# Performance work log

Hardware: AMD Instinct MI355X
Metric: run time of the kernel (lower is better)

Reference implementation:

```python
import jax, jax.numpy as jnp
import numpy as np

N = 30000   # nodes
E = 300000  # edges
B = 64      # graphs
H = 4       # heads
C = 64      # channels per head
HC = H * C  # 256


def setup_inputs() -> dict:
    key = jax.random.key(0)
    ks = jax.random.split(key, 32)

    def rn(k, shape):
        scale = 1.0 / np.sqrt(shape[0])
        return (jax.random.normal(k, shape) * scale).astype(jnp.float32)

    inp = {}
    inp["x"] = jax.random.normal(ks[0], (N, 13), dtype=jnp.float32)
    inp["edge_index"] = jax.random.randint(ks[1], (2, E), 0, N, dtype=jnp.int64)
    inp["edge_attr"] = jax.random.normal(ks[2], (E, 51), dtype=jnp.float32)
    inp["batch"] = jnp.sort(jax.random.randint(ks[3], (N,), 0, B, dtype=jnp.int64))
    # init node MLP: Linear(13 -> 128) (plain_last => no act/norm)
    inp["W0"] = rn(ks[4], (13, 128)); inp["b0"] = jnp.zeros((128,), jnp.float32)
    # GATv2 layer 1: in 128 -> H=4, C=64
    inp["Wl1"] = rn(ks[5], (128, HC)); inp["bl1"] = jnp.zeros((HC,), jnp.float32)
    inp["Wr1"] = rn(ks[6], (128, HC)); inp["br1"] = jnp.zeros((HC,), jnp.float32)
    inp["We1"] = rn(ks[7], (51, HC))
    inp["att1"] = rn(ks[8], (H, C))
    inp["bias1"] = jnp.zeros((HC,), jnp.float32)
    # GATv2 layer 2: in 256 -> H=4, C=64
    inp["Wl2"] = rn(ks[9], (HC, HC)); inp["bl2"] = jnp.zeros((HC,), jnp.float32)
    inp["Wr2"] = rn(ks[10], (HC, HC)); inp["br2"] = jnp.zeros((HC,), jnp.float32)
    inp["We2"] = rn(ks[11], (51, HC))
    inp["att2"] = rn(ks[12], (H, C))
    inp["bias2"] = jnp.zeros((HC,), jnp.float32)
    # attention pooling MLP: Linear(256 -> 256) (plain_last)
    inp["Wp"] = rn(ks[13], (HC, HC)); inp["bp"] = jnp.zeros((HC,), jnp.float32)
    # out MLP: Linear(256->256)+BN+ReLU, Linear(256->2001)
    inp["Wo1"] = rn(ks[14], (HC, 256)); inp["bo1"] = jnp.zeros((256,), jnp.float32)
    inp["gamma"] = jnp.ones((256,), jnp.float32); inp["beta"] = jnp.zeros((256,), jnp.float32)
    inp["Wo2"] = rn(ks[15], (256, 2001)); inp["bo2"] = jnp.zeros((2001,), jnp.float32)
    return inp


def _gatv2(x, src, dst, ea, Wl, bl, Wr, br, We, att, bias):
    n = x.shape[0]
    xl = (x @ Wl + bl).reshape(n, H, C)   # source transform (also message content)
    xr = (x @ Wr + br).reshape(n, H, C)   # target transform
    ee = (ea @ We).reshape(-1, H, C)      # edge embedding, no bias
    z = jax.nn.leaky_relu(xl[src] + xr[dst] + ee, negative_slope=0.2)  # [E,H,C]
    logit = jnp.einsum('ehc,hc->eh', z, att)                           # [E,H]
    m = jax.ops.segment_max(logit, dst, num_segments=n)                # [N,H]
    w = jnp.exp(logit - m[dst])
    den = jax.ops.segment_sum(w, dst, num_segments=n)
    alpha = w / (den[dst] + 1e-16)                                     # segment softmax
    out = jax.ops.segment_sum(xl[src] * alpha[:, :, None], dst, num_segments=n)
    return out.reshape(n, HC) + bias


def _forward(x, edge_index, edge_attr, batch, W0, b0, Wl1, bl1, Wr1, br1, We1, att1, bias1,
             Wl2, bl2, Wr2, br2, We2, att2, bias2, Wp, bp, Wo1, bo1, gamma, beta, Wo2, bo2):
    src, dst = edge_index[0], edge_index[1]
    h = x @ W0 + b0
    h = _gatv2(h, src, dst, edge_attr, Wl1, bl1, Wr1, br1, We1, att1, bias1)
    h = _gatv2(h, src, dst, edge_attr, Wl2, bl2, Wr2, br2, We2, att2, bias2)
    # softmax attention pooling over nodes of each graph (per feature column)
    a = h @ Wp + bp                                       # [N,HC]
    am = jax.ops.segment_max(a, batch, num_segments=B)
    aw = jnp.exp(a - am[batch])
    ad = jax.ops.segment_sum(aw, batch, num_segments=B)
    attw = aw / (ad[batch] + 1e-16)
    g = jax.ops.segment_sum(h * attw, batch, num_segments=B)  # [B,HC]
    # out MLP: Linear + BatchNorm(train stats) + ReLU + Linear, then leaky_relu
    y = g @ Wo1 + bo1
    mu = jnp.mean(y, axis=0)
    var = jnp.var(y, axis=0)
    y = (y - mu) / jnp.sqrt(var + 1e-5) * gamma + beta
    y = jax.nn.relu(y)
    y = y @ Wo2 + bo2
    return jax.nn.leaky_relu(y, negative_slope=0.01)


def reference(x, edge_index, edge_attr, batch, W0, b0, Wl1, bl1, Wr1, br1, We1, att1, bias1,
              Wl2, bl2, Wr2, br2, We2, att2, bias2, Wp, bp, Wo1, bo1, gamma, beta, Wo2, bo2):
    return _forward(x, edge_index, edge_attr, batch, W0, b0, Wl1, bl1, Wr1, br1, We1, att1, bias1,
                    Wl2, bl2, Wr2, br2, We2, att2, bias2, Wp, bp, Wo1, bo1, gamma, beta, Wo2, bo2)
```

## Files before the change

### kernel.cpp

```cpp
#include <hip/hip_runtime.h>
#include <hip/hip_bf16.h>

#define NN 30000
#define EE 300000
#define BB 64
#define HH 4
#define CC 64
#define HC 256

typedef __attribute__((ext_vector_type(8))) short short8;
typedef __attribute__((ext_vector_type(4))) float floatx4;

__device__ __forceinline__ float b2f(short x) {
    return __uint_as_float(((unsigned)(unsigned short)x) << 16);
}
__device__ __forceinline__ unsigned short f2b(float f) {
    __hip_bfloat16 h = __float2bfloat16(f);
    return *(unsigned short*)&h;
}

#define GLD16(gp, lp) __builtin_amdgcn_global_load_lds( \
    (const __attribute__((address_space(1))) void*)(gp), \
    (__attribute__((address_space(3))) void*)(lp), 16, 0, 0)

#define ROT2(x) ((((x) << 2) | ((x) >> 3)) & 31)

template<int CT>
__global__ __launch_bounds__(256) void mfma_gemm(
    const ushort* __restrict__ A, const ushort* __restrict__ Bt,
    const float* __restrict__ bias, float* __restrict__ outF,
    __hip_bfloat16* __restrict__ outB, int M, int Nc, int K) {
    __shared__ __align__(16) ushort lA[64 * 32];
    __shared__ __align__(16) ushort lB[CT * 64 * 32];
    const int tid = threadIdx.x, lane = tid & 63, wv = tid >> 6;
    const int row0 = blockIdx.x * 64, col0 = blockIdx.y * (CT * 64);

    floatx4 acc[4][CT];
#pragma unroll
    for (int r = 0; r < 4; r++)
#pragma unroll
        for (int c = 0; c < CT; c++) acc[r][c] = (floatx4){0.f, 0.f, 0.f, 0.f};

    const int arow = tid >> 2;
    const int sl   = (tid & 3) ^ ((tid >> 3) & 3);
    const ushort* ga = A + (size_t)(row0 + arow) * K + sl * 8;
    const int m16 = lane & 15, q = lane >> 4;

    for (int k0 = 0; k0 < K; k0 += 32) {
        __syncthreads();
        GLD16(ga + k0, &lA[tid * 8]);
#pragma unroll
        for (int j = 0; j < CT; j++) {
            const ushort* gb = Bt + (size_t)(col0 + j * 64 + arow) * K + k0 + sl * 8;
            GLD16(gb, &lB[j * 2048 + tid * 8]);
        }
        __syncthreads();
        short8 aF[4], bF[CT];
#pragma unroll
        for (int r = 0; r < 4; r++) {
            int rr = r * 16 + m16;
            aF[r] = *(const short8*)&lA[rr * 32 + ((q ^ ((rr >> 1) & 3)) << 3)];
        }
#pragma unroll
        for (int c = 0; c < CT; c++) {
            int nr = (wv * CT + c) * 16 + m16;
            bF[c] = *(const short8*)&lB[nr * 32 + ((q ^ ((nr >> 1) & 3)) << 3)];
        }
#pragma unroll
        for (int r = 0; r < 4; r++)
#pragma unroll
            for (int c = 0; c < CT; c++)
                acc[r][c] = __builtin_amdgcn_mfma_f32_16x16x32_bf16(aF[r], bF[c], acc[r][c], 0, 0, 0);
    }

#pragma unroll
    for (int c = 0; c < CT; c++) {
        int col = col0 + (wv * CT + c) * 16 + m16;
        float bv = bias ? bias[col] : 0.f;
#pragma unroll
        for (int r = 0; r < 4; r++)
#pragma unroll
            for (int j = 0; j < 4; j++) {
                int row = row0 + r * 16 + q * 4 + j;
                if (row < M) {
                    float v = acc[r][c][j] + bv;
                    if (outB) outB[(size_t)row * Nc + col] = __float2bfloat16(v);
                    else      outF[(size_t)row * Nc + col] = v;
                }
            }
    }
}

__global__ void permute_ea_frag(const float* __restrict__ ea,
                                const int* __restrict__ eidx,
                                ushort* __restrict__ ea_frag) {
    const int t = threadIdx.x, tile = blockIdx.x;
    const int r  = t >> 6;
    const int ch = (t >> 3) & 7;
    const int m0 = (t * 2) & 15;
    ushort* outp = ea_frag + (size_t)tile * 4096 + t * 16;
#pragma unroll
    for (int half = 0; half < 2; half++) {
        int row = r * 16 + m0 + half;
        int gi = tile * 64 + row;
        int e = (gi < EE) ? eidx[gi] : -1;
        short8 v8;
#pragma unroll
        for (int j = 0; j < 8; j++) {
            int k = ch * 8 + j;
            float v = (e >= 0 && k < 51) ? ea[(size_t)e * 51 + k] : 0.f;
            v8[j] = (short)f2b(v);
        }
        *(short8*)(outp + half * 8) = v8;
    }
}

__global__ void pack_we_frag(const float* __restrict__ WeA,
                             const float* __restrict__ WeB,
                             ushort* __restrict__ WfA, ushort* __restrict__ WfB) {
    const float* We = blockIdx.y ? WeB : WeA;
    ushort* Wf = blockIdx.y ? WfB : WfA;
    int o = blockIdx.x * 256 + threadIdx.x;
    int j = o & 7, m16 = (o >> 3) & 15, ch = (o >> 7) & 7, nt = o >> 10;
    int n = nt * 16 + m16, k = ch * 8 + j;
    float v = (k < 51) ? We[k * 256 + n] : 0.f;
    Wf[o] = f2b(v);
}

__global__ __launch_bounds__(256, 4) void edge_fused(
    const ushort* __restrict__ ea_frag, const ushort* __restrict__ Wfrag,
    const float* __restrict__ att,
    const int* __restrict__ src_csr, const int* __restrict__ dst_csr,
    const ushort* __restrict__ xlr, float* __restrict__ logitp) {
    __shared__ __align__(16) ushort eeS[64 * 256];
    __shared__ float satt[256];
    const int tid = threadIdx.x, lane = tid & 63, wv = tid >> 6;
    const int i0 = blockIdx.x * 64;
    satt[tid] = att[tid];
    const int m16 = lane & 15, q = lane >> 4;

    floatx4 acc[4][4];
#pragma unroll
    for (int r = 0; r < 4; r++)
#pragma unroll
        for (int c = 0; c < 4; c++) acc[r][c] = (floatx4){0.f, 0.f, 0.f, 0.f};

    const ushort* af = ea_frag + (size_t)blockIdx.x * 4096;
#pragma unroll
    for (int k0 = 0; k0 < 2; k0++) {
        short8 aF[4], bF[4];
#pragma unroll
        for (int r = 0; r < 4; r++)
            aF[r] = *(const short8*)&af[((r * 8 + k0 * 4 + q) * 16 + m16) * 8];
#pragma unroll
        for (int c = 0; c < 4; c++)
            bF[c] = *(const short8*)&Wfrag[(((wv * 4 + c) * 8 + k0 * 4 + q) * 16 + m16) * 8];
#pragma unroll
        for (int r = 0; r < 4; r++)
#pragma unroll
            for (int c = 0; c < 4; c++)
                acc[r][c] = __builtin_amdgcn_mfma_f32_16x16x32_bf16(aF[r], bF[c], acc[r][c], 0, 0, 0);
    }

#pragma unroll
    for (int r = 0; r < 4; r++)
#pragma unroll
        for (int cc = 0; cc < 4; cc++)
#pragma unroll
            for (int j = 0; j < 4; j++) {
                int row = r * 16 + q * 4 + j;
                int col = (wv * 4 + cc) * 16 + m16;
                int chunk = col >> 3;
                int P = ROT2(chunk) ^ ((row >> 2) & 3);
                eeS[row * 256 + (P << 3) + (col & 7)] = f2b(acc[r][cc][j]);
            }
    __syncthreads();

    const int el = tid >> 2, h = tid & 3;
    const int i = i0 + el;
    if (i < EE) {
        int src = src_csr[i], dstn = dst_csr[i];
        const ushort* xlp = xlr + (size_t)src * 512 + h * 64;
        const ushort* xrp = xlr + (size_t)dstn * 512 + 256 + h * 64;
        float s = 0.f;
#pragma unroll
        for (int c = 0; c < 8; c++) {
            short8 xlv = *(const short8*)(xlp + c * 8);
            short8 xrv = *(const short8*)(xrp + c * 8);
            int chunk = h * 8 + c;
            int P = ROT2(chunk) ^ ((el >> 2) & 3);
            short8 eev = *(const short8*)&eeS[el * 256 + (P << 3)];
#pragma unroll
            for (int j = 0; j < 8; j++) {
                float v = b2f(xlv[j]) + b2f(xrv[j]) + b2f(eev[j]);
                v = v > 0.f ? v : 0.2f * v;
                s += v * satt[h * 64 + c * 8 + j];
            }
        }
        logitp[(size_t)i * 4 + h] = s;
    }
}

__global__ void pack_x(const float* __restrict__ x, __hip_bfloat16* __restrict__ d) {
    int i = blockIdx.x * 256 + threadIdx.x;
    if (i >= NN * 32) return;
    int n = i >> 5, k = i & 31;
    d[i] = __float2bfloat16(k < 13 ? x[n * 13 + k] : 0.f);
}
struct PackJob { const float* W; __hip_bfloat16* dst; int K, Nc, Kpad, rowoff; };
struct PackJobs { PackJob j[6]; };
__global__ void pack_all(PackJobs jobs) {
    PackJob jb = jobs.j[blockIdx.y];
    int tot = jb.Nc * jb.Kpad;
    for (int i = blockIdx.x * 256 + threadIdx.x; i < tot; i += gridDim.x * 256) {
        int n = i / jb.Kpad, k = i - n * jb.Kpad;
        float v = (k < jb.K) ? jb.W[k * jb.Nc + n] : 0.f;
        jb.dst[(size_t)(jb.rowoff + n) * jb.Kpad + k] = __float2bfloat16(v);
    }
}
__global__ void cat2(const float* __restrict__ a, const float* __restrict__ b,
                     float* __restrict__ o) {
    int i = blockIdx.x * 256 + threadIdx.x;
    if (i < 512) o[i] = i < 256 ? a[i] : b[i - 256];
}

__global__ void hist_deg(const int* __restrict__ ei, int* __restrict__ deg) {
    int e = blockIdx.x * 256 + threadIdx.x;
    if (e < EE) atomicAdd(&deg[ei[EE + e]], 1);
}
__global__ void scan1(const int* __restrict__ deg, int* __restrict__ partial,
                      int* __restrict__ bsum) {
    __shared__ int sh[256];
    int t = threadIdx.x, i = blockIdx.x * 256 + t;
    int v = (i < NN) ? deg[i] : 0;
    sh[t] = v; __syncthreads();
    for (int off = 1; off < 256; off <<= 1) {
        int x = (t >= off) ? sh[t - off] : 0;
        __syncthreads();
        sh[t] += x;
        __syncthreads();
    }
    if (i < NN) partial[i] = sh[t] - v;
    if (t == 255) bsum[blockIdx.x] = sh[255];
}
__global__ void scan2(int* __restrict__ bsum, int nb) {
    __shared__ int sh[256];
    int t = threadIdx.x;
    int v = (t < nb) ? bsum[t] : 0;
    sh[t] = v; __syncthreads();
    for (int off = 1; off < 256; off <<= 1) {
        int x = (t >= off) ? sh[t - off] : 0;
        __syncthreads();
        sh[t] += x;
        __syncthreads();
    }
    if (t < nb) bsum[t] = sh[t] - v;
}
__global__ void scan3(const int* __restrict__ partial, const int* __restrict__ bsum,
                      int* __restrict__ start) {
    int i = blockIdx.x * 256 + threadIdx.x;
    if (i < NN) start[i] = partial[i] + bsum[i >> 8];
    else if (i == NN) start[NN] = EE;
}
__global__ void scatter_e(const int* __restrict__ ei, int* __restrict__ cursor,
                          const int* __restrict__ start, int* __restrict__ eidx,
                          int* __restrict__ src_csr, int* __restrict__ dst_csr) {
    int e = blockIdx.x * 256 + threadIdx.x;
    if (e >= EE) return;
    int s = ei[e];
    int d = ei[EE + e];
    int p = atomicAdd(&cursor[d], 1);
    int pos = start[d] + p;
    eidx[pos] = e;
    src_csr[pos] = s;
    dst_csr[pos] = d;
}

__global__ __launch_bounds__(256) void aggregate_csr(
    const ushort* __restrict__ xlr, const float* __restrict__ logitp,
    const int* __restrict__ src_csr, const int* __restrict__ start,
    const float* __restrict__ bias, ushort* __restrict__ outb) {
    const int lane = threadIdx.x & 63, wv = threadIdx.x >> 6;
    const int dst = blockIdx.x * 4 + wv;
    if (dst >= NN) return;
    const int s0 = start[dst];
    const int deg = start[dst + 1] - s0;
    const int h = lane >> 4;

    float m[4] = {-3.4e38f, -3.4e38f, -3.4e38f, -3.4e38f};
    float lg[4] = {0.f, 0.f, 0.f, 0.f};
    int mysrc = 0;
    if (lane < deg) {
        mysrc = src_csr[s0 + lane];
        float4 l4 = ((const float4*)logitp)[s0 + lane];
        lg[0] = l4.x; lg[1] = l4.y; lg[2] = l4.z; lg[3] = l4.w;
        m[0] = l4.x; m[1] = l4.y; m[2] = l4.z; m[3] = l4.w;
    }
    for (int i = 64 + lane; i < deg; i += 64) {
        float4 l4 = ((const float4*)logitp)[s0 + i];
        m[0] = fmaxf(m[0], l4.x); m[1] = fmaxf(m[1], l4.y);
        m[2] = fmaxf(m[2], l4.z); m[3] = fmaxf(m[3], l4.w);
    }
#pragma unroll
    for (int off = 32; off; off >>= 1)
#pragma unroll
        for (int k = 0; k < 4; k++) m[k] = fmaxf(m[k], __shfl_xor(m[k], off));

    float w[4], d[4];
#pragma unroll
    for (int k = 0; k < 4; k++) {
        w[k] = (lane < deg) ? __expf(lg[k] - m[k]) : 0.f;
        d[k] = w[k];
    }
    for (int i = 64 + lane; i < deg; i += 64) {
        float4 l4 = ((const float4*)logitp)[s0 + i];
        d[0] += __expf(l4.x - m[0]); d[1] += __expf(l4.y - m[1]);
        d[2] += __expf(l4.z - m[2]); d[3] += __expf(l4.w - m[3]);
    }
#pragma unroll
    for (int off = 32; off; off >>= 1)
#pragma unroll
        for (int k = 0; k < 4; k++) d[k] += __shfl_xor(d[k], off);
    const float dh = 1.f / (((h == 0) ? d[0] : (h == 1) ? d[1] : (h == 2) ? d[2] : d[3]) + 1e-16f);
    const float mh = (h == 0) ? m[0] : (h == 1) ? m[1] : (h == 2) ? m[2] : m[3];

    float4 b4 = ((const float4*)bias)[lane];
    float a0 = b4.x, a1 = b4.y, a2 = b4.z, a3 = b4.w;

    const int dcap = deg < 64 ? deg : 64;
    for (int i = 0; i < dcap; i++) {
        int srcv = __shfl(mysrc, i);
        float s0v = __shfl(w[0], i), s1v = __shfl(w[1], i);
        float s2v = __shfl(w[2], i), s3v = __shfl(w[3], i);
        float aw = ((h == 0) ? s0v : (h == 1) ? s1v : (h == 2) ? s2v : s3v) * dh;
        ushort4 xv = *(const ushort4*)(xlr + (size_t)srcv * 512 + lane * 4);
        a0 += b2f(xv.x) * aw; a1 += b2f(xv.y) * aw;
        a2 += b2f(xv.z) * aw; a3 += b2f(xv.w) * aw;
    }
    for (int i = 64; i < deg; i++) {
        int srcv = src_csr[s0 + i];
        float4 l4 = ((const float4*)logitp)[s0 + i];
        float lh = (h == 0) ? l4.x : (h == 1) ? l4.y : (h == 2) ? l4.z : l4.w;
        float aw = __expf(lh - mh) * dh;
        ushort4 xv = *(const ushort4*)(xlr + (size_t)srcv * 512 + lane * 4);
        a0 += b2f(xv.x) * aw; a1 += b2f(xv.y) * aw;
        a2 += b2f(xv.z) * aw; a3 += b2f(xv.w) * aw;
    }
    ushort4 ov;
    ov.x = f2b(a0); ov.y = f2b(a1); ov.z = f2b(a2); ov.w = f2b(a3);
    *(ushort4*)(outb + (size_t)dst * 256 + lane * 4) = ov;
}

__device__ __forceinline__ unsigned fmap(float f) {
    unsigned u = __float_as_uint(f);
    return (u & 0x80000000u) ? ~u : (u | 0x80000000u);
}
__device__ __forceinline__ float funmap(unsigned u) {
    return (u & 0x80000000u) ? __uint_as_float(u & 0x7FFFFFFFu)
                             : __uint_as_float(~u);
}

__global__ void pool_max(const float* __restrict__ a, const int* __restrict__ batch,
                         unsigned* __restrict__ am) {
    const int c = threadIdx.x;
    const int n0 = blockIdx.x * 64;
    int curb = batch[n0];
    float m = -3.4e38f;
    const int nend = min(n0 + 64, NN);
    for (int n = n0; n < nend; n++) {
        int b = batch[n];
        float v = a[(size_t)n * HC + c];
        if (b != curb) { atomicMax(&am[curb * HC + c], fmap(m)); curb = b; m = v; }
        else           { m = fmaxf(m, v); }
    }
    atomicMax(&am[curb * HC + c], fmap(m));
}
__global__ void pool_sums(const float* __restrict__ a, const __hip_bfloat16* __restrict__ h2,
                          const int* __restrict__ batch, const unsigned* __restrict__ am,
                          float* __restrict__ den, float* __restrict__ num) {
    const int c = threadIdx.x;
    const int n0 = blockIdx.x * 64;
    int curb = batch[n0];
    float sd = 0.f, sn = 0.f;
    float mcur = funmap(am[curb * HC + c]);
    const int nend = min(n0 + 64, NN);
    for (int n = n0; n < nend; n++) {
        int b = batch[n];
        if (b != curb) {
            atomicAdd(&den[curb * HC + c], sd);
            atomicAdd(&num[curb * HC + c], sn);
            curb = b; sd = 0.f; sn = 0.f; mcur = funmap(am[b * HC + c]);
        }
        float w = __expf(a[(size_t)n * HC + c] - mcur);
        sd += w;
        sn += __bfloat162float(h2[(size_t)n * HC + c]) * w;
    }
    atomicAdd(&den[curb * HC + c], sd);
    atomicAdd(&num[curb * HC + c], sn);
}
__global__ void pool_div(const float* __restrict__ num, const float* __restrict__ den,
                         float* __restrict__ g) {
    int i = blockIdx.x * 256 + threadIdx.x;
    g[i] = num[i] / (den[i] + 1e-16f);
}

__global__ void mlp_lin1(const float* __restrict__ g, const float* __restrict__ Wo1,
                         const float* __restrict__ bo1, float* __restrict__ y) {
    const int c = threadIdx.x;
    const int r = blockIdx.x;
    float acc = bo1[c];
#pragma unroll 4
    for (int k = 0; k < HC; k++) acc = fmaf(g[r * HC + k], Wo1[k * HC + c], acc);
    y[r * HC + c] = acc;
}
__global__ void bn_relu(float* __restrict__ y, const float* __restrict__ gamma,
                        const float* __restrict__ beta) {
    const int c = threadIdx.x;
    float s = 0.f, sq = 0.f;
    for (int r = 0; r < BB; r++) { float v = y[r * HC + c]; s += v; sq += v * v; }
    float mu  = s * (1.f / BB);
    float var = sq * (1.f / BB) - mu * mu;
    float inv = rsqrtf(var + 1e-5f) * gamma[c];
    float bt  = beta[c];
    for (int r = 0; r < BB; r++) {
        float v = (y[r * HC + c] - mu) * inv + bt;
        y[r * HC + c] = v > 0.f ? v : 0.f;
    }
}
__global__ void mlp_lin2(const float* __restrict__ y, const float* __restrict__ Wo2,
                         const float* __restrict__ bo2, float* __restrict__ out) {
    const int j = blockIdx.x * 256 + threadIdx.x;
    const int r = blockIdx.y;
    if (j >= 2001) return;
    float acc = bo2[j];
#pragma unroll 4
    for (int k = 0; k < HC; k++) acc = fmaf(y[r * HC + k], Wo2[k * 2001 + j], acc);
    out[r * 2001 + j] = acc > 0.f ? acc : 0.01f * acc;
}

extern "C" void kernel_launch(void* const* d_in, const int* in_sizes, int n_in,
                              void* d_out, int out_size, void* d_ws, size_t ws_size,
                              hipStream_t stream) {
    const float* x     = (const float*)d_in[0];
    const int*   ei    = (const int*)d_in[1];
    const float* ea    = (const float*)d_in[2];
    const int*   batch = (const int*)d_in[3];
    const float* W0 = (const float*)d_in[4];  const float* b0 = (const float*)d_in[5];
    const float* Wl1 = (const float*)d_in[6]; const float* bl1 = (const float*)d_in[7];
    const float* Wr1 = (const float*)d_in[8]; const float* br1 = (const float*)d_in[9];
    const float* We1 = (const float*)d_in[10]; const float* att1 = (const float*)d_in[11];
    const float* bias1 = (const float*)d_in[12];
    const float* Wl2 = (const float*)d_in[13]; const float* bl2 = (const float*)d_in[14];
    const float* Wr2 = (const float*)d_in[15]; const float* br2 = (const float*)d_in[16];
    const float* We2 = (const float*)d_in[17]; const float* att2 = (const float*)d_in[18];
    const float* bias2 = (const float*)d_in[19];
    const float* Wp = (const float*)d_in[20]; const float* bp = (const float*)d_in[21];
    const float* Wo1 = (const float*)d_in[22]; const float* bo1 = (const float*)d_in[23];
    const float* gamma = (const float*)d_in[24]; const float* beta = (const float*)d_in[25];
    const float* Wo2 = (const float*)d_in[26]; const float* bo2 = (const float*)d_in[27];
    float* out = (float*)d_out;

    char* p = (char*)d_ws;
    auto alloc = [&](size_t bytes) { char* r = p; p += (bytes + 255) & ~(size_t)255; return r; };
    const int MP = 30016;
    const int ET = 4688;
    __hip_bfloat16* xpad  = (__hip_bfloat16*)alloc((size_t)MP * 32 * 2);
    __hip_bfloat16* W0t   = (__hip_bfloat16*)alloc(128 * 32 * 2);
    __hip_bfloat16* W1t   = (__hip_bfloat16*)alloc(512 * 128 * 2);
    __hip_bfloat16* W2t   = (__hip_bfloat16*)alloc(512 * 256 * 2);
    __hip_bfloat16* Wpt   = (__hip_bfloat16*)alloc(256 * 256 * 2);
    ushort* Wef1 = (ushort*)alloc(256 * 64 * 2);
    ushort* Wef2 = (ushort*)alloc(256 * 64 * 2);
    float* bcat1 = (float*)alloc(512 * 4);
    float* bcat2 = (float*)alloc(512 * 4);
    __hip_bfloat16* h0b  = (__hip_bfloat16*)alloc((size_t)MP * 128 * 2);
    __hip_bfloat16* xlrb = (__hip_bfloat16*)alloc((size_t)MP * 512 * 2);
    __hip_bfloat16* h1b  = (__hip_bfloat16*)alloc((size_t)MP * 256 * 2);
    __hip_bfloat16* h2b  = (__hip_bfloat16*)alloc((size_t)MP * 256 * 2);
    ushort* ea_frag = (ushort*)alloc((size_t)ET * 4096 * 2);
    float* abuf = (float*)alloc((size_t)MP * 256 * 4);
    float* logit = (float*)alloc((size_t)EE * 4 * 4);
    int* deg    = (int*)alloc(NN * 4);
    int* cursor = (int*)alloc(NN * 4);
    int* partial= (int*)alloc(NN * 4);
    int* bsum   = (int*)alloc(256 * 4);
    int* start  = (int*)alloc((NN + 4) * 4);
    int* eidx   = (int*)alloc((size_t)EE * 4);
    int* src_csr= (int*)alloc((size_t)EE * 4);
    int* dst_csr= (int*)alloc((size_t)EE * 4);
    unsigned* am = (unsigned*)alloc(BB * HC * 4);
    float* den  = (float*)alloc(BB * HC * 4);
    float* num  = (float*)alloc(BB * HC * 4);
    float* g    = (float*)alloc(BB * HC * 4);
    float* ybuf = (float*)alloc(BB * HC * 4);

    const int NB = (NN + 255) / 256;

    pack_x<<<(NN * 32 + 255) / 256, 256, 0, stream>>>(x, xpad);
    PackJobs pj;
    pj.j[0] = {W0,  W0t, 13, 128, 32, 0};
    pj.j[1] = {Wl1, W1t, 128, 256, 128, 0};
    pj.j[2] = {Wr1, W1t, 128, 256, 128, 256};
    pj.j[3] = {Wl2, W2t, 256, 256, 256, 0};
    pj.j[4] = {Wr2, W2t, 256, 256, 256, 256};
    pj.j[5] = {Wp,  Wpt, 256, 256, 256, 0};
    pack_all<<<dim3(64, 6), 256, 0, stream>>>(pj);
    pack_we_frag<<<dim3(64, 2), 256, 0, stream>>>(We1, We2, Wef1, Wef2);
    cat2<<<2, 256, 0, stream>>>(bl1, br1, bcat1);
    cat2<<<2, 256, 0, stream>>>(bl2, br2, bcat2);

    hipMemsetAsync(deg, 0, NN * 4, stream);
    hipMemsetAsync(cursor, 0, NN * 4, stream);
    hist_deg<<<(EE + 255) / 256, 256, 0, stream>>>(ei, deg);
    scan1<<<NB, 256, 0, stream>>>(deg, partial, bsum);
    scan2<<<1, 256, 0, stream>>>(bsum, NB);
    scan3<<<NB + 1, 256, 0, stream>>>(partial, bsum, start);
    scatter_e<<<(EE + 255) / 256, 256, 0, stream>>>(ei, cursor, start, eidx, src_csr, dst_csr);
    permute_ea_frag<<<ET, 256, 0, stream>>>(ea, eidx, ea_frag);

    mfma_gemm<2><<<dim3(469, 1), 256, 0, stream>>>(
        (const ushort*)xpad, (const ushort*)W0t, b0, nullptr, h0b, NN, 128, 32);

    mfma_gemm<4><<<dim3(469, 2), 256, 0, stream>>>(
        (const ushort*)h0b, (const ushort*)W1t, bcat1, nullptr, xlrb, NN, 512, 128);
    edge_fused<<<ET, 256, 0, stream>>>(ea_frag, Wef1, att1, src_csr, dst_csr,
                                       (const ushort*)xlrb, logit);
    aggregate_csr<<<(NN + 3) / 4, 256, 0, stream>>>(
        (const ushort*)xlrb, logit, src_csr, start, bias1, (ushort*)h1b);

    mfma_gemm<4><<<dim3(469, 2), 256, 0, stream>>>(
        (const ushort*)h1b, (const ushort*)W2t, bcat2, nullptr, xlrb, NN, 512, 256);
    edge_fused<<<ET, 256, 0, stream>>>(ea_frag, Wef2, att2, src_csr, dst_csr,
                                       (const ushort*)xlrb, logit);
    aggregate_csr<<<(NN + 3) / 4, 256, 0, stream>>>(
        (const ushort*)xlrb, logit, src_csr, start, bias2, (ushort*)h2b);

    mfma_gemm<4><<<dim3(469, 1), 256, 0, stream>>>(
        (const ushort*)h2b, (const ushort*)Wpt, bp, abuf, nullptr, NN, 256, 256);
    hipMemsetAsync(am, 0, BB * HC * 4, stream);
    hipMemsetAsync(den, 0, BB * HC * 4, stream);
    hipMemsetAsync(num, 0, BB * HC * 4, stream);
    const int poolGrid = (NN + 63) / 64;
    pool_max<<<poolGrid, HC, 0, stream>>>(abuf, batch, am);
    pool_sums<<<poolGrid, HC, 0, stream>>>(abuf, h2b, batch, am, den, num);
    pool_div<<<BB, HC, 0, stream>>>(num, den, g);

    mlp_lin1<<<BB, HC, 0, stream>>>(g, Wo1, bo1, ybuf);
    bn_relu<<<1, HC, 0, stream>>>(ybuf, gamma, beta);
    mlp_lin2<<<dim3(8, BB), 256, 0, stream>>>(ybuf, Wo2, bo2, out);
}
```

Measured before the change: 646.4 us.

## Fold memsets and pool_div into kernels, unroll aggregate gather, refine LDS swizzle

The memsets for deg, cursor, den and num are replaced by zeroing inside kernels that already run (pack_x, scan3, pool_max), and pool_div is fused into mlp_lin1 through shared memory. This cuts launch and memset overhead. The aggregate loop is unrolled by four so that four independent gathers are in flight at once, hiding memory latency. The edge_fused LDS swizzle gains an extra XOR term to reduce bank conflicts. Zeroing den and num inside pool_max works only because stream order places it before pool_sums. The unrolling adds register pressure.

New measurement: 627.2 us. 1.03x faster.

```diff
diff --git a/kernel.cpp b/kernel.cpp
--- a/kernel.cpp
+++ b/kernel.cpp
@@ -24,6 +24,7 @@
     (__attribute__((address_space(3))) void*)(lp), 16, 0, 0)
 
 #define ROT2(x) ((((x) << 2) | ((x) >> 3)) & 31)
+#define EESWZ(chunk, row) (ROT2(chunk) ^ (((row) >> 2) & 3) ^ (((row) & 1) << 2))
 
 template<int CT>
 __global__ __launch_bounds__(256) void mfma_gemm(
@@ -171,7 +172,7 @@
                 int row = r * 16 + q * 4 + j;
                 int col = (wv * 4 + cc) * 16 + m16;
                 int chunk = col >> 3;
-                int P = ROT2(chunk) ^ ((row >> 2) & 3);
+                int P = EESWZ(chunk, row);
                 eeS[row * 256 + (P << 3) + (col & 7)] = f2b(acc[r][cc][j]);
             }
     __syncthreads();
@@ -188,7 +189,7 @@
             short8 xlv = *(const short8*)(xlp + c * 8);
             short8 xrv = *(const short8*)(xrp + c * 8);
             int chunk = h * 8 + c;
-            int P = ROT2(chunk) ^ ((el >> 2) & 3);
+            int P = EESWZ(chunk, el);
             short8 eev = *(const short8*)&eeS[el * 256 + (P << 3)];
 #pragma unroll
             for (int j = 0; j < 8; j++) {
@@ -201,8 +202,10 @@
     }
 }
 
-__global__ void pack_x(const float* __restrict__ x, __hip_bfloat16* __restrict__ d) {
+__global__ void pack_x(const float* __restrict__ x, __hip_bfloat16* __restrict__ d,
+                       int* __restrict__ deg) {
     int i = blockIdx.x * 256 + threadIdx.x;
+    if (i < NN) deg[i] = 0;
     if (i >= NN * 32) return;
     int n = i >> 5, k = i & 31;
     d[i] = __float2bfloat16(k < 13 ? x[n * 13 + k] : 0.f);
@@ -257,9 +260,9 @@
     if (t < nb) bsum[t] = sh[t] - v;
 }
 __global__ void scan3(const int* __restrict__ partial, const int* __restrict__ bsum,
-                      int* __restrict__ start) {
+                      int* __restrict__ start, int* __restrict__ cursor) {
     int i = blockIdx.x * 256 + threadIdx.x;
-    if (i < NN) start[i] = partial[i] + bsum[i >> 8];
+    if (i < NN) { start[i] = partial[i] + bsum[i >> 8]; cursor[i] = 0; }
     else if (i == NN) start[NN] = EE;
 }
 __global__ void scatter_e(const int* __restrict__ ei, int* __restrict__ cursor,
@@ -328,21 +331,42 @@
     float a0 = b4.x, a1 = b4.y, a2 = b4.z, a3 = b4.w;
 
     const int dcap = deg < 64 ? deg : 64;
-    for (int i = 0; i < dcap; i++) {
+    const ushort* xbase = xlr + (size_t)lane * 4;
+    int i = 0;
+    for (; i + 4 <= dcap; i += 4) {
+        int sv[4]; float aw[4];
+#pragma unroll
+        for (int u = 0; u < 4; u++) {
+            sv[u] = __shfl(mysrc, i + u);
+            float s0v = __shfl(w[0], i + u), s1v = __shfl(w[1], i + u);
+            float s2v = __shfl(w[2], i + u), s3v = __shfl(w[3], i + u);
+            aw[u] = ((h == 0) ? s0v : (h == 1) ? s1v : (h == 2) ? s2v : s3v) * dh;
+        }
+        ushort4 xv[4];
+#pragma unroll
+        for (int u = 0; u < 4; u++)
+            xv[u] = *(const ushort4*)(xbase + (size_t)sv[u] * 512);
+#pragma unroll
+        for (int u = 0; u < 4; u++) {
+            a0 += b2f(xv[u].x) * aw[u]; a1 += b2f(xv[u].y) * aw[u];
+            a2 += b2f(xv[u].z) * aw[u]; a3 += b2f(xv[u].w) * aw[u];
+        }
+    }
+    for (; i < dcap; i++) {
         int srcv = __shfl(mysrc, i);
         float s0v = __shfl(w[0], i), s1v = __shfl(w[1], i);
         float s2v = __shfl(w[2], i), s3v = __shfl(w[3], i);
         float aw = ((h == 0) ? s0v : (h == 1) ? s1v : (h == 2) ? s2v : s3v) * dh;
-        ushort4 xv = *(const ushort4*)(xlr + (size_t)srcv * 512 + lane * 4);
+        ushort4 xv = *(const ushort4*)(xbase + (size_t)srcv * 512);
         a0 += b2f(xv.x) * aw; a1 += b2f(xv.y) * aw;
         a2 += b2f(xv.z) * aw; a3 += b2f(xv.w) * aw;
     }
-    for (int i = 64; i < deg; i++) {
-        int srcv = src_csr[s0 + i];
-        float4 l4 = ((const float4*)logitp)[s0 + i];
+    for (int ii = 64; ii < deg; ii++) {
+        int srcv = src_csr[s0 + ii];
+        float4 l4 = ((const float4*)logitp)[s0 + ii];
         float lh = (h == 0) ? l4.x : (h == 1) ? l4.y : (h == 2) ? l4.z : l4.w;
         float aw = __expf(lh - mh) * dh;
-        ushort4 xv = *(const ushort4*)(xlr + (size_t)srcv * 512 + lane * 4);
+        ushort4 xv = *(const ushort4*)(xbase + (size_t)srcv * 512);
         a0 += b2f(xv.x) * aw; a1 += b2f(xv.y) * aw;
         a2 += b2f(xv.z) * aw; a3 += b2f(xv.w) * aw;
     }
@@ -361,8 +385,13 @@
 }
 
 __global__ void pool_max(const float* __restrict__ a, const int* __restrict__ batch,
-                         unsigned* __restrict__ am) {
+                         unsigned* __restrict__ am, float* __restrict__ den,
+                         float* __restrict__ num) {
     const int c = threadIdx.x;
+    if (blockIdx.x < BB) {
+        den[blockIdx.x * HC + c] = 0.f;
+        num[blockIdx.x * HC + c] = 0.f;
+    }
     const int n0 = blockIdx.x * 64;
     int curb = batch[n0];
     float m = -3.4e38f;
@@ -398,19 +427,18 @@
     atomicAdd(&den[curb * HC + c], sd);
     atomicAdd(&num[curb * HC + c], sn);
 }
-__global__ void pool_div(const float* __restrict__ num, const float* __restrict__ den,
-                         float* __restrict__ g) {
-    int i = blockIdx.x * 256 + threadIdx.x;
-    g[i] = num[i] / (den[i] + 1e-16f);
-}
-
-__global__ void mlp_lin1(const float* __restrict__ g, const float* __restrict__ Wo1,
-                         const float* __restrict__ bo1, float* __restrict__ y) {
+
+__global__ void mlp_lin1(const float* __restrict__ num, const float* __restrict__ den,
+                         const float* __restrict__ Wo1, const float* __restrict__ bo1,
+                         float* __restrict__ y) {
+    __shared__ float gsh[HC];
     const int c = threadIdx.x;
     const int r = blockIdx.x;
+    gsh[c] = num[r * HC + c] / (den[r * HC + c] + 1e-16f);
+    __syncthreads();
     float acc = bo1[c];
 #pragma unroll 4
-    for (int k = 0; k < HC; k++) acc = fmaf(g[r * HC + k], Wo1[k * HC + c], acc);
+    for (int k = 0; k < HC; k++) acc = fmaf(gsh[k], Wo1[k * HC + c], acc);
     y[r * HC + c] = acc;
 }
 __global__ void bn_relu(float* __restrict__ y, const float* __restrict__ gamma,
@@ -491,12 +519,11 @@
     unsigned* am = (unsigned*)alloc(BB * HC * 4);
     float* den  = (float*)alloc(BB * HC * 4);
     float* num  = (float*)alloc(BB * HC * 4);
-    float* g    = (float*)alloc(BB * HC * 4);
     float* ybuf = (float*)alloc(BB * HC * 4);
 
     const int NB = (NN + 255) / 256;
 
-    pack_x<<<(NN * 32 + 255) / 256, 256, 0, stream>>>(x, xpad);
+    pack_x<<<(NN * 32 + 255) / 256, 256, 0, stream>>>(x, xpad, deg);
     PackJobs pj;
     pj.j[0] = {W0,  W0t, 13, 128, 32, 0};
     pj.j[1] = {Wl1, W1t, 128, 256, 128, 0};
@@ -509,12 +536,10 @@
     cat2<<<2, 256, 0, stream>>>(bl1, br1, bcat1);
     cat2<<<2, 256, 0, stream>>>(bl2, br2, bcat2);
 
-    hipMemsetAsync(deg, 0, NN * 4, stream);
-    hipMemsetAsync(cursor, 0, NN * 4, stream);
     hist_deg<<<(EE + 255) / 256, 256, 0, stream>>>(ei, deg);
     scan1<<<NB, 256, 0, stream>>>(deg, partial, bsum);
     scan2<<<1, 256, 0, stream>>>(bsum, NB);
-    scan3<<<NB + 1, 256, 0, stream>>>(partial, bsum, start);
+    scan3<<<NB + 1, 256, 0, stream>>>(partial, bsum, start, cursor);
     scatter_e<<<(EE + 255) / 256, 256, 0, stream>>>(ei, cursor, start, eidx, src_csr, dst_csr);
     permute_ea_frag<<<ET, 256, 0, stream>>>(ea, eidx, ea_frag);
 
@@ -538,14 +563,11 @@
     mfma_gemm<4><<<dim3(469, 1), 256, 0, stream>>>(
         (const ushort*)h2b, (const ushort*)Wpt, bp, abuf, nullptr, NN, 256, 256);
     hipMemsetAsync(am, 0, BB * HC * 4, stream);
-    hipMemsetAsync(den, 0, BB * HC * 4, stream);
-    hipMemsetAsync(num, 0, BB * HC * 4, stream);
     const int poolGrid = (NN + 63) / 64;
-    pool_max<<<poolGrid, HC, 0, stream>>>(abuf, batch, am);
+    pool_max<<<poolGrid, HC, 0, stream>>>(abuf, batch, am, den, num);
     pool_sums<<<poolGrid, HC, 0, stream>>>(abuf, h2b, batch, am, den, num);
-    pool_div<<<BB, HC, 0, stream>>>(num, den, g);
-
-    mlp_lin1<<<BB, HC, 0, stream>>>(g, Wo1, bo1, ybuf);
+
+    mlp_lin1<<<BB, HC, 0, stream>>>(num, den, Wo1, bo1, ybuf);
     bn_relu<<<1, HC, 0, stream>>>(ybuf, gamma, beta);
     mlp_lin2<<<dim3(8, BB), 256, 0, stream>>>(ybuf, Wo2, bo2, out);
 }
```
